# Optimization experiments

Hardware: AMD Instinct MI355X
Metric: run time of the kernel (lower is better)

The kernel has to match this reference:

```python
import jax, jax.numpy as jnp
import numpy as np

B, OUT, IN = 2048, 4096, 4096
KEEPRATE = 0.5  # mid-training drop schedule state; first-call default masks nothing


def setup_inputs() -> dict:
    key = jax.random.key(0)
    k1, k2, k3, k4 = jax.random.split(key, 4)
    data = jax.random.normal(k1, (B, IN), dtype=jnp.float32)
    # weight parameter = fftn of a real N(0, 0.1) matrix, stored as complex
    w0 = jax.random.normal(k2, (OUT, IN), dtype=jnp.float32) * 0.1
    wc = jnp.fft.fftn(w0.astype(jnp.float32))
    w_real = jnp.real(wc).astype(jnp.float32)
    w_imag = jnp.imag(wc).astype(jnp.float32)
    bias = jax.random.normal(k3, (OUT,), dtype=jnp.float32) * 0.1
    # ZMAT: rank assignment, a permutation of 0..OUT*IN-1
    zmat = jax.random.permutation(k4, jnp.arange(OUT * IN, dtype=jnp.int64)).reshape(OUT, IN)
    return {"data": data, "w_real": w_real, "w_imag": w_imag, "bias": bias, "zmat": zmat}


def reference(data, w_real, w_imag, bias, zmat):
    O, I = w_real.shape
    numel = O * I
    threval = KEEPRATE * numel
    # IDROP: keep entries whose rank <= threshold (ZMAT > threval -> 0)
    idrop = (zmat.astype(jnp.float32) <= threval).astype(w_real.dtype)
    dropweight = (w_real + 1j * w_imag) * idrop  # masked FFT-domain weight
    # torch.fft.irfftn(dropweight, s=(O, I)): full ifft on dim 0, real irfft on dim 1
    # (numpy/jax irfft crops the last axis to I//2+1, same as torch)
    w_spatial = jnp.fft.irfftn(dropweight, s=(O, I), axes=(0, 1)).astype(data.dtype)
    return data @ w_spatial.T + bias
```

## Files before the change

kernel.cpp:

```cpp
#include <hip/hip_runtime.h>
#include <hip/hip_bf16.h>
#include <stdint.h>

#define OUT_N 4096
#define IN_N  4096
#define BATCH 2048
#define KHALF 2049

typedef __bf16 bf16x8 __attribute__((ext_vector_type(8)));
typedef float  f32x4  __attribute__((ext_vector_type(4)));

__device__ __forceinline__ unsigned short f2bf(float f) {
  unsigned int u = __builtin_bit_cast(unsigned int, f);
  u += 0x7FFFu + ((u >> 16) & 1u);
  return (unsigned short)(u >> 16);
}

__device__ __forceinline__ float2 cmul(float2 a, float2 b) {
  return make_float2(a.x * b.x - a.y * b.y, a.x * b.y + a.y * b.x);
}
__device__ __forceinline__ float2 cadd(float2 a, float2 b) { return make_float2(a.x + b.x, a.y + b.y); }
__device__ __forceinline__ float2 csub(float2 a, float2 b) { return make_float2(a.x - b.x, a.y - b.y); }
__device__ __forceinline__ float2 muli(float2 a) { return make_float2(-a.y, a.x); }

__device__ __forceinline__ void dft4i(float2& x0, float2& x1, float2& x2, float2& x3) {
  float2 t0 = cadd(x0, x2), t1 = csub(x0, x2);
  float2 t2 = cadd(x1, x3), t3 = csub(x1, x3);
  float2 it3 = muli(t3);
  x0 = cadd(t0, t2); x2 = csub(t0, t2);
  x1 = cadd(t1, it3); x3 = csub(t1, it3);
}

#define C8f  0.70710678118654752f
#define C16f 0.92387953251128676f
#define S16f 0.38268343236508977f

__device__ __forceinline__ void dft16i(float2 r[16]) {
  float2 t[16];
#pragma unroll
  for (int b = 0; b < 4; ++b) {
    float2 a0 = r[b], a1 = r[4 + b], a2 = r[8 + b], a3 = r[12 + b];
    dft4i(a0, a1, a2, a3);
    t[b * 4 + 0] = a0; t[b * 4 + 1] = a1; t[b * 4 + 2] = a2; t[b * 4 + 3] = a3;
  }
  const float2 W1 = make_float2(C16f, S16f);
  const float2 W2 = make_float2(C8f, C8f);
  const float2 W3 = make_float2(S16f, C16f);
  const float2 W6 = make_float2(-C8f, C8f);
  const float2 W9 = make_float2(-C16f, -S16f);
  t[5]  = cmul(t[5],  W1);  t[6]  = cmul(t[6],  W2);  t[7]  = cmul(t[7],  W3);
  t[9]  = cmul(t[9],  W2);  t[10] = muli(t[10]);      t[11] = cmul(t[11], W6);
  t[13] = cmul(t[13], W3);  t[14] = cmul(t[14], W6);  t[15] = cmul(t[15], W9);
#pragma unroll
  for (int q = 0; q < 4; ++q) {
    float2 a0 = t[q], a1 = t[4 + q], a2 = t[8 + q], a3 = t[12 + q];
    dft4i(a0, a1, a2, a3);
    r[q] = a0; r[q + 4] = a1; r[q + 8] = a2; r[q + 12] = a3;
  }
}

__device__ __forceinline__ void twiddle16(float2 r[16], float theta) {
  float sn, cs;
  __sincosf(theta, &sn, &cs);
  float2 w = make_float2(cs, sn);
  float2 wk = w;
  r[1] = cmul(r[1], wk);
#pragma unroll
  for (int k = 2; k < 16; ++k) {
    wk = cmul(wk, w);
    r[k] = cmul(r[k], wk);
  }
}

__device__ void fft4096_core(float2 r[16], float2* lds, int t) {
  dft16i(r);
  twiddle16(r, 1.53398078788564123e-3f * (float)t);
#pragma unroll
  for (int k1 = 0; k1 < 16; ++k1) lds[k1 * 257 + t] = r[k1];
  __syncthreads();
  const int k1 = t & 15, b = t >> 4;
  float2 s[16];
#pragma unroll
  for (int a = 0; a < 16; ++a) s[a] = lds[k1 * 257 + 16 * a + b];
  __syncthreads();
  dft16i(s);
  twiddle16(s, 2.45436926061702596e-2f * (float)b);
#pragma unroll
  for (int c = 0; c < 16; ++c) lds[k1 * 273 + c * 17 + b] = s[c];
  __syncthreads();
#pragma unroll
  for (int bb = 0; bb < 16; ++bb) r[bb] = lds[k1 * 273 + b * 17 + bb];
  dft16i(r);
}

__global__ void mask_transpose(const float* __restrict__ wr, const float* __restrict__ wi,
                               const int* __restrict__ zmat, float2* __restrict__ wt) {
  __shared__ float2 tile[32][65];
  const int tx = threadIdx.x;
  const int ty = threadIdx.y;
  const int o0 = blockIdx.y * 32;
  if (blockIdx.x == 32) {
    int t = ty * 32 + tx;
    if (t < 32) {
      int o = o0 + t;
      size_t idx = (size_t)o * IN_N + 2048;
      float2 v = make_float2(0.f, 0.f);
      if (zmat[idx] <= 8388608) v = make_float2(wr[idx], wi[idx]);
      wt[(size_t)2048 * OUT_N + o] = v;
    }
    return;
  }
  const int k0 = blockIdx.x * 64;
#pragma unroll
  for (int r = 0; r < 4; ++r) {
    int o = o0 + ty + r * 8;
    size_t base = (size_t)o * IN_N + k0 + tx * 2;
    float2 vr = *(const float2*)&wr[base];
    float2 vi = *(const float2*)&wi[base];
    int2   z  = *(const int2*)&zmat[base];
    tile[ty + r * 8][tx * 2]     = (z.x <= 8388608) ? make_float2(vr.x, vi.x) : make_float2(0.f, 0.f);
    tile[ty + r * 8][tx * 2 + 1] = (z.y <= 8388608) ? make_float2(vr.y, vi.y) : make_float2(0.f, 0.f);
  }
  __syncthreads();
#pragma unroll
  for (int rr = 0; rr < 8; ++rr) {
    int k = k0 + ty + rr * 8;
    int o = o0 + tx;
    wt[(size_t)k * OUT_N + o] = tile[tx][ty + rr * 8];
  }
}

__global__ __launch_bounds__(256) void col_ifft(float2* __restrict__ wt) {
  __shared__ float2 lds[4368];
  const int t = threadIdx.x;
  float2* row = wt + (size_t)blockIdx.x * OUT_N;
  float2 r[16];
#pragma unroll
  for (int n1 = 0; n1 < 16; ++n1) r[n1] = row[n1 * 256 + t];
  fft4096_core(r, lds, t);
#pragma unroll
  for (int d = 0; d < 16; ++d) row[t + 256 * d] = r[d];
}

__global__ void transpose_ko(const float2* __restrict__ yt, float2* __restrict__ y) {
  __shared__ float2 tile[32][33];
  const int k0 = blockIdx.x * 32;
  const int o0 = blockIdx.y * 32;
  const int tx = threadIdx.x;
  const int ty = threadIdx.y;
#pragma unroll
  for (int r = 0; r < 4; ++r) {
    int k = k0 + ty + r * 8;
    int o = o0 + tx;
    if (k < KHALF) tile[ty + r * 8][tx] = yt[(size_t)k * OUT_N + o];
  }
  __syncthreads();
#pragma unroll
  for (int r = 0; r < 4; ++r) {
    int o = o0 + ty + r * 8;
    int k = k0 + tx;
    if (k < KHALF) y[(size_t)o * KHALF + k] = tile[tx][ty + r * 8];
  }
}

__global__ __launch_bounds__(256) void row_irfft2(const float2* __restrict__ y,
                                                  unsigned short* __restrict__ wbf) {
  __shared__ float2 lds[4368];
  const int t = threadIdx.x;
  const int oa = blockIdx.x * 2, ob = oa + 1;
  const float2* rowa = y + (size_t)oa * KHALF;
  const float2* rowb = y + (size_t)ob * KHALF;
  float2* lsa = lds;
  float2* lsb = lds + 2049;
#pragma unroll
  for (int j = 0; j < 9; ++j) {
    int k = t + j * 256;
    if (k < KHALF) { lsa[k] = rowa[k]; lsb[k] = rowb[k]; }
  }
  __syncthreads();
  float2 r[16];
#pragma unroll
  for (int n1 = 0; n1 < 16; ++n1) {
    int m = n1 * 256 + t;
    float2 za, zb;
    if (m == 0)        { za = make_float2(lsa[0].x, 0.f);    zb = make_float2(lsb[0].x, 0.f); }
    else if (m < 2048) { za = lsa[m];                        zb = lsb[m]; }
    else if (m == 2048){ za = make_float2(lsa[2048].x, 0.f); zb = make_float2(lsb[2048].x, 0.f); }
    else { float2 ua = lsa[4096 - m], ub = lsb[4096 - m];
           za = make_float2(ua.x, -ua.y); zb = make_float2(ub.x, -ub.y); }
    r[n1] = make_float2(za.x - zb.y, za.y + zb.x);
  }
  __syncthreads();
  fft4096_core(r, lds, t);
  const float sc = 1.0f / (4096.0f * 4096.0f);
  unsigned short* orow_a = wbf + (size_t)oa * IN_N;
  unsigned short* orow_b = wbf + (size_t)ob * IN_N;
#pragma unroll
  for (int d = 0; d < 16; ++d) {
    orow_a[t + 256 * d] = f2bf(r[d].x * sc);
    orow_b[t + 256 * d] = f2bf(r[d].y * sc);
  }
}

__global__ void cvt_bf16(const float* __restrict__ x, unsigned short* __restrict__ o, int n4) {
  int i = blockIdx.x * blockDim.x + threadIdx.x;
  if (i < n4) {
    float4 v = ((const float4*)x)[i];
    ushort4 r;
    r.x = f2bf(v.x); r.y = f2bf(v.y); r.z = f2bf(v.z); r.w = f2bf(v.w);
    ((ushort4*)o)[i] = r;
  }
}

#define BK 64

__device__ __forceinline__ void gload_lds16(const void* gp, void* lp) {
  typedef const __attribute__((address_space(1))) void* gptr_t;
  typedef __attribute__((address_space(3))) void* lptr_t;
  __builtin_amdgcn_global_load_lds((gptr_t)(unsigned long long)gp,
                                   (lptr_t)(unsigned int)(unsigned long long)lp,
                                   16, 0, 0);
}

__global__ __launch_bounds__(256) void gemm_bt_bias(const unsigned short* __restrict__ A,
                                                    const unsigned short* __restrict__ B,
                                                    const float* __restrict__ bias,
                                                    float* __restrict__ C) {
  __shared__ __align__(16) unsigned short As[128 * BK];
  __shared__ __align__(16) unsigned short Bs[128 * BK];
  const int tid  = threadIdx.x;
  const int wave = tid >> 6;
  const int lane = tid & 63;
  const int gm0 = blockIdx.y * 128;
  const int gn0 = blockIdx.x * 128;

  f32x4 acc[4][4] = {};
  const int wm = wave >> 1, wn = wave & 1;
  const int srow   = lane >> 3;
  const int schunk = (lane & 7) ^ srow;
  const int l7 = lane & 7;
  const int qbase = lane >> 4;
  const int fra = wm * 64 + (lane & 15);
  const int frb = wn * 64 + (lane & 15);

  for (int kt = 0; kt < IN_N; kt += BK) {
#pragma unroll
    for (int j = 0; j < 4; ++j) {
      const int r0 = wave * 32 + j * 8;
      gload_lds16(A + ((size_t)(gm0 + r0 + srow) * IN_N + kt + schunk * 8),
                  As + (size_t)r0 * BK);
      gload_lds16(B + ((size_t)(gn0 + r0 + srow) * IN_N + kt + schunk * 8),
                  Bs + (size_t)r0 * BK);
    }
    __syncthreads();

#pragma unroll
    for (int kk = 0; kk < 2; ++kk) {
      bf16x8 af[4], bfr[4];
      const int q = kk * 4 + qbase;
#pragma unroll
      for (int i = 0; i < 4; ++i) {
        af[i]  = *(const bf16x8*)&As[(fra + i * 16) * BK + (q ^ l7) * 8];
        bfr[i] = *(const bf16x8*)&Bs[(frb + i * 16) * BK + (q ^ l7) * 8];
      }
#pragma unroll
      for (int mi = 0; mi < 4; ++mi)
#pragma unroll
        for (int ni = 0; ni < 4; ++ni)
          acc[mi][ni] = __builtin_amdgcn_mfma_f32_16x16x32_bf16(af[mi], bfr[ni], acc[mi][ni], 0, 0, 0);
    }
    __syncthreads();
  }

  const int col0 = gn0 + wn * 64 + (lane & 15);
  const int row0 = gm0 + wm * 64 + (lane >> 4) * 4;
#pragma unroll
  for (int mi = 0; mi < 4; ++mi) {
#pragma unroll
    for (int ni = 0; ni < 4; ++ni) {
      int col = col0 + ni * 16;
      float bv = bias[col];
#pragma unroll
      for (int r = 0; r < 4; ++r) {
        int row = row0 + mi * 16 + r;
        C[(size_t)row * OUT_N + col] = acc[mi][ni][r] + bv;
      }
    }
  }
}

extern "C" void kernel_launch(void* const* d_in, const int* in_sizes, int n_in,
                              void* d_out, int out_size, void* d_ws, size_t ws_size,
                              hipStream_t stream) {
  const float* data = (const float*)d_in[0];
  const float* wr   = (const float*)d_in[1];
  const float* wi   = (const float*)d_in[2];
  const float* bias = (const float*)d_in[3];
  const int*   zmat = (const int*)d_in[4];

  char* ws = (char*)d_ws;
  float2* wt = (float2*)ws;
  float2* y  = (float2*)(ws + 67141632ull);
  unsigned short* wbf = (unsigned short*)ws;
  unsigned short* dbf = (unsigned short*)(ws + 33554432ull);

  hipLaunchKernelGGL(mask_transpose, dim3(33, 128), dim3(32, 8), 0, stream, wr, wi, zmat, wt);
  hipLaunchKernelGGL(col_ifft,       dim3(2049),    dim3(256),   0, stream, wt);
  hipLaunchKernelGGL(transpose_ko,   dim3(65, 128), dim3(32, 8), 0, stream, wt, y);
  hipLaunchKernelGGL(row_irfft2,     dim3(2048),    dim3(256),   0, stream, y, wbf);
  hipLaunchKernelGGL(cvt_bf16,       dim3(8192),    dim3(256),   0, stream, data, dbf, (BATCH * IN_N) / 4);
  hipLaunchKernelGGL(gemm_bt_bias,   dim3(OUT_N / 128, BATCH / 128), dim3(256), 0, stream,
                     dbf, wbf, bias, (float*)d_out);
}
```

Baseline: 367.0 us.

## Double-buffer GEMM LDS tiles and XOR-swizzle FFT shared memory

The bf16 GEMM now keeps two LDS stages. The tile for step t+2 is issued with global_load_lds while step t is being computed, using explicit vmcnt waits and s_barrier in place of __syncthreads. The FFT kernels replace padded LDS indexing with an XOR swizzle, which cuts LDS to 4096 float2 and allows a launch bound of 5 blocks per CU. The Nyquist element in row_irfft2 is now read straight from global memory. The GEMM change doubles LDS use and depends on hand-counted vmcnt values being correct.

```diff
diff --git a/kernel.cpp b/kernel.cpp
--- a/kernel.cpp
+++ b/kernel.cpp
@@ -76,20 +76,20 @@
   dft16i(r);
   twiddle16(r, 1.53398078788564123e-3f * (float)t);
 #pragma unroll
-  for (int k1 = 0; k1 < 16; ++k1) lds[k1 * 257 + t] = r[k1];
+  for (int k1 = 0; k1 < 16; ++k1) lds[k1 * 256 + (t ^ k1)] = r[k1];
   __syncthreads();
   const int k1 = t & 15, b = t >> 4;
   float2 s[16];
 #pragma unroll
-  for (int a = 0; a < 16; ++a) s[a] = lds[k1 * 257 + 16 * a + b];
+  for (int a = 0; a < 16; ++a) s[a] = lds[k1 * 256 + ((16 * a + b) ^ k1)];
   __syncthreads();
   dft16i(s);
   twiddle16(s, 2.45436926061702596e-2f * (float)b);
 #pragma unroll
-  for (int c = 0; c < 16; ++c) lds[k1 * 273 + c * 17 + b] = s[c];
-  __syncthreads();
-#pragma unroll
-  for (int bb = 0; bb < 16; ++bb) r[bb] = lds[k1 * 273 + b * 17 + bb];
+  for (int c = 0; c < 16; ++c) lds[k1 * 256 + ((c * 16 + b) ^ k1)] = s[c];
+  __syncthreads();
+#pragma unroll
+  for (int bb = 0; bb < 16; ++bb) r[bb] = lds[k1 * 256 + ((b * 16 + bb) ^ k1)];
   dft16i(r);
 }
 
@@ -130,8 +130,8 @@
   }
 }
 
-__global__ __launch_bounds__(256) void col_ifft(float2* __restrict__ wt) {
-  __shared__ float2 lds[4368];
+__global__ __launch_bounds__(256, 5) void col_ifft(float2* __restrict__ wt) {
+  __shared__ float2 lds[4096];
   const int t = threadIdx.x;
   float2* row = wt + (size_t)blockIdx.x * OUT_N;
   float2 r[16];
@@ -163,19 +163,19 @@
   }
 }
 
-__global__ __launch_bounds__(256) void row_irfft2(const float2* __restrict__ y,
-                                                  unsigned short* __restrict__ wbf) {
-  __shared__ float2 lds[4368];
+__global__ __launch_bounds__(256, 5) void row_irfft2(const float2* __restrict__ y,
+                                                     unsigned short* __restrict__ wbf) {
+  __shared__ float2 lds[4096];
   const int t = threadIdx.x;
   const int oa = blockIdx.x * 2, ob = oa + 1;
   const float2* rowa = y + (size_t)oa * KHALF;
   const float2* rowb = y + (size_t)ob * KHALF;
   float2* lsa = lds;
-  float2* lsb = lds + 2049;
-#pragma unroll
-  for (int j = 0; j < 9; ++j) {
+  float2* lsb = lds + 2048;
+#pragma unroll
+  for (int j = 0; j < 8; ++j) {
     int k = t + j * 256;
-    if (k < KHALF) { lsa[k] = rowa[k]; lsb[k] = rowb[k]; }
+    lsa[k] = rowa[k]; lsb[k] = rowb[k];
   }
   __syncthreads();
   float2 r[16];
@@ -185,7 +185,8 @@
     float2 za, zb;
     if (m == 0)        { za = make_float2(lsa[0].x, 0.f);    zb = make_float2(lsb[0].x, 0.f); }
     else if (m < 2048) { za = lsa[m];                        zb = lsb[m]; }
-    else if (m == 2048){ za = make_float2(lsa[2048].x, 0.f); zb = make_float2(lsb[2048].x, 0.f); }
+    else if (m == 2048){ float2 na = rowa[2048], nb = rowb[2048];
+                         za = make_float2(na.x, 0.f);        zb = make_float2(nb.x, 0.f); }
     else { float2 ua = lsa[4096 - m], ub = lsb[4096 - m];
            za = make_float2(ua.x, -ua.y); zb = make_float2(ub.x, -ub.y); }
     r[n1] = make_float2(za.x - zb.y, za.y + zb.x);
@@ -213,6 +214,7 @@
 }
 
 #define BK 64
+#define NT (IN_N / BK)
 
 __device__ __forceinline__ void gload_lds16(const void* gp, void* lp) {
   typedef const __attribute__((address_space(1))) void* gptr_t;
@@ -222,12 +224,26 @@
                                    16, 0, 0);
 }
 
+__device__ __forceinline__ void stage_tile(const unsigned short* __restrict__ A,
+                                           const unsigned short* __restrict__ B,
+                                           unsigned short* as, unsigned short* bs,
+                                           int gm0, int gn0, int kt,
+                                           int r0, int srow, int schunk) {
+#pragma unroll
+  for (int j = 0; j < 4; ++j) {
+    gload_lds16(A + ((size_t)(gm0 + r0 + j * 8 + srow) * IN_N + kt + schunk * 8),
+                as + (size_t)(r0 + j * 8) * BK);
+    gload_lds16(B + ((size_t)(gn0 + r0 + j * 8 + srow) * IN_N + kt + schunk * 8),
+                bs + (size_t)(r0 + j * 8) * BK);
+  }
+}
+
 __global__ __launch_bounds__(256) void gemm_bt_bias(const unsigned short* __restrict__ A,
                                                     const unsigned short* __restrict__ B,
                                                     const float* __restrict__ bias,
                                                     float* __restrict__ C) {
-  __shared__ __align__(16) unsigned short As[128 * BK];
-  __shared__ __align__(16) unsigned short Bs[128 * BK];
+  __shared__ __align__(16) unsigned short As[2][128 * BK];
+  __shared__ __align__(16) unsigned short Bs[2][128 * BK];
   const int tid  = threadIdx.x;
   const int wave = tid >> 6;
   const int lane = tid & 63;
@@ -238,21 +254,22 @@
   const int wm = wave >> 1, wn = wave & 1;
   const int srow   = lane >> 3;
   const int schunk = (lane & 7) ^ srow;
+  const int r0     = wave * 32;
   const int l7 = lane & 7;
   const int qbase = lane >> 4;
   const int fra = wm * 64 + (lane & 15);
   const int frb = wn * 64 + (lane & 15);
 
-  for (int kt = 0; kt < IN_N; kt += BK) {
-#pragma unroll
-    for (int j = 0; j < 4; ++j) {
-      const int r0 = wave * 32 + j * 8;
-      gload_lds16(A + ((size_t)(gm0 + r0 + srow) * IN_N + kt + schunk * 8),
-                  As + (size_t)r0 * BK);
-      gload_lds16(B + ((size_t)(gn0 + r0 + srow) * IN_N + kt + schunk * 8),
-                  Bs + (size_t)r0 * BK);
-    }
-    __syncthreads();
+  stage_tile(A, B, As[0], Bs[0], gm0, gn0, 0,  r0, srow, schunk);
+  stage_tile(A, B, As[1], Bs[1], gm0, gn0, BK, r0, srow, schunk);
+
+  for (int t = 0; t < NT; ++t) {
+    const int S = t & 1;
+    if (t < NT - 1) asm volatile("s_waitcnt vmcnt(8)" ::: "memory");
+    else            asm volatile("s_waitcnt vmcnt(0)" ::: "memory");
+    __builtin_amdgcn_sched_barrier(0);
+    __builtin_amdgcn_s_barrier();
+    __builtin_amdgcn_sched_barrier(0);
 
 #pragma unroll
     for (int kk = 0; kk < 2; ++kk) {
@@ -260,8 +277,8 @@
       const int q = kk * 4 + qbase;
 #pragma unroll
       for (int i = 0; i < 4; ++i) {
-        af[i]  = *(const bf16x8*)&As[(fra + i * 16) * BK + (q ^ l7) * 8];
-        bfr[i] = *(const bf16x8*)&Bs[(frb + i * 16) * BK + (q ^ l7) * 8];
+        af[i]  = *(const bf16x8*)&As[S][(fra + i * 16) * BK + ((q ^ l7) * 8)];
+        bfr[i] = *(const bf16x8*)&Bs[S][(frb + i * 16) * BK + ((q ^ l7) * 8)];
       }
 #pragma unroll
       for (int mi = 0; mi < 4; ++mi)
@@ -269,7 +286,10 @@
         for (int ni = 0; ni < 4; ++ni)
           acc[mi][ni] = __builtin_amdgcn_mfma_f32_16x16x32_bf16(af[mi], bfr[ni], acc[mi][ni], 0, 0, 0);
     }
-    __syncthreads();
+    __builtin_amdgcn_sched_barrier(0);
+    __builtin_amdgcn_s_barrier();
+    if (t + 2 < NT)
+      stage_tile(A, B, As[S], Bs[S], gm0, gn0, (t + 2) * BK, r0, srow, schunk);
   }
 
   const int col0 = gn0 + wn * 64 + (lane & 15);
```

New measurement: 403.2 us. 9.9% more time.
